# Performance work log

Measured on AMD Instinct MI355X. Metric: run time of the kernel, lower is better.

## Reference

```python
import jax, jax.numpy as jnp
import numpy as np
import math

IN_DIM = 2048
OUT_DIM = 2048
BATCH = 4096
BN_EPS = 1e-5


def setup_inputs() -> dict:
    key = jax.random.key(0)
    ks = jax.random.split(key, 6)
    x = jax.random.normal(ks[0], (BATCH, IN_DIM), dtype=jnp.float32)
    # scale ~ N(1.0, 0.1), translate = 0
    scale = 1.0 + 0.1 * jax.random.normal(ks[1], (1, IN_DIM), dtype=jnp.float32)
    translate = jnp.zeros((1, IN_DIM), dtype=jnp.float32)
    # kaiming-normal-ish init for wave_weight (fan_in), orthogonal-ish for base_weight
    wave_weight = jax.random.normal(ks[2], (OUT_DIM, IN_DIM), dtype=jnp.float32) * np.sqrt(2.0 / IN_DIM)
    bw = jax.random.normal(ks[3], (OUT_DIM, IN_DIM), dtype=jnp.float32)
    q, _ = jnp.linalg.qr(bw.T)  # (IN_DIM, OUT_DIM) orthonormal columns
    base_weight = q.T.astype(jnp.float32)
    gamma = jnp.ones((OUT_DIM,), dtype=jnp.float32)
    beta = jnp.zeros((OUT_DIM,), dtype=jnp.float32)
    return {"x": x, "scale": scale, "translate": translate,
            "wave_weight": wave_weight, "base_weight": base_weight,
            "gamma": gamma, "beta": beta}


def reference(x, scale, translate, wave_weight, base_weight, gamma, beta):
    # Bio wavelet: pi^-1/4 * cos(3u) * exp(-0.5 u^2), u = (x - t) / clamp(s, 1e-3)
    u = (x - translate) / jnp.maximum(scale, 1e-3)            # (B, in)
    wavelet = (math.pi ** -0.25) * jnp.cos(3.0 * u) * jnp.exp(-0.5 * u * u)
    # einsum 'boi,oi->bo' with singleton o broadcast == plain matmul
    wave_out = jnp.einsum('bi,oi->bo', wavelet, wave_weight)  # (B, out)
    base_out = jnp.einsum('bi,oi->bo', x, base_weight)        # (B, out)
    y = wave_out + 0.3 * base_out
    # BatchNorm1d (training mode: batch statistics, biased variance)
    mean = jnp.mean(y, axis=0)
    var = jnp.mean(jnp.square(y - mean), axis=0)
    out = gamma * (y - mean) * jax.lax.rsqrt(var + BN_EPS) + beta
    # dropout treated as identity (deterministic reference)
    return out
```

## Files before the change

### kernel.cpp

```cpp
#include <hip/hip_runtime.h>
#include <stdint.h>

#define IN_DIM 2048
#define OUT_DIM 2048
#define BATCH 4096
#define KDIM (2 * IN_DIM)
#define KROWB (KDIM * 2)
#define KH 2048
#define BN_EPS 1e-5f

typedef __attribute__((ext_vector_type(8))) short bf16x8;
typedef __attribute__((ext_vector_type(4))) float f32x4;

__device__ __forceinline__ unsigned short f2bf(float f) {
  union { float f; unsigned u; } v; v.f = f;
  unsigned r = v.u + 0x7FFFu + ((v.u >> 16) & 1u);
  return (unsigned short)(r >> 16);
}

__global__ void prep_act(const float* __restrict__ x,
                         const float* __restrict__ scale,
                         const float* __restrict__ translate,
                         unsigned short* __restrict__ A) {
  int e = (blockIdx.x * 256 + threadIdx.x) * 4;
  int b = e / IN_DIM;
  int i = e % IN_DIM;
  float4 xv = *(const float4*)(x + e);
  float4 sv = *(const float4*)(scale + i);
  float4 tv = *(const float4*)(translate + i);
  const float c = 0.7511255444649425f;
  float u0 = (xv.x - tv.x) / fmaxf(sv.x, 1e-3f);
  float u1 = (xv.y - tv.y) / fmaxf(sv.y, 1e-3f);
  float u2 = (xv.z - tv.z) / fmaxf(sv.z, 1e-3f);
  float u3 = (xv.w - tv.w) / fmaxf(sv.w, 1e-3f);
  ushort4 wv, xb;
  wv.x = f2bf(c * __cosf(3.0f * u0) * __expf(-0.5f * u0 * u0));
  wv.y = f2bf(c * __cosf(3.0f * u1) * __expf(-0.5f * u1 * u1));
  wv.z = f2bf(c * __cosf(3.0f * u2) * __expf(-0.5f * u2 * u2));
  wv.w = f2bf(c * __cosf(3.0f * u3) * __expf(-0.5f * u3 * u3));
  xb.x = f2bf(xv.x); xb.y = f2bf(xv.y); xb.z = f2bf(xv.z); xb.w = f2bf(xv.w);
  *(ushort4*)(A + (size_t)b * KDIM + i) = wv;
  *(ushort4*)(A + (size_t)b * KDIM + IN_DIM + i) = xb;
}

__global__ void prep_w(const float* __restrict__ ww,
                       const float* __restrict__ bw,
                       unsigned short* __restrict__ W) {
  int e = (blockIdx.x * 256 + threadIdx.x) * 4;
  int o = e / IN_DIM;
  int k = e % IN_DIM;
  float4 a = *(const float4*)(ww + e);
  float4 b = *(const float4*)(bw + e);
  ushort4 wa, wb;
  wa.x = f2bf(a.x); wa.y = f2bf(a.y); wa.z = f2bf(a.z); wa.w = f2bf(a.w);
  wb.x = f2bf(0.3f * b.x); wb.y = f2bf(0.3f * b.y);
  wb.z = f2bf(0.3f * b.z); wb.w = f2bf(0.3f * b.w);
  *(ushort4*)(W + (size_t)o * KDIM + k) = wa;
  *(ushort4*)(W + (size_t)o * KDIM + IN_DIM + k) = wb;
}


#define GLDS(gp, lo) __builtin_amdgcn_global_load_lds( \
    (const __attribute__((address_space(1))) void*)(gp), \
    (__attribute__((address_space(3))) void*)(lds + (lo) + ldsl), 16, 0, 0)

#define MM16(mh) do { \
  __builtin_amdgcn_s_setprio(1); \
  _Pragma("unroll") for (int i2 = 0; i2 < 4; ++i2) \
  _Pragma("unroll") for (int j2 = 0; j2 < 4; ++j2) \
    acc[(mh) * 4 + i2][j2] = __builtin_amdgcn_mfma_f32_16x16x32_bf16( \
        af[i2], bfr[j2], acc[(mh) * 4 + i2][j2], 0, 0, 0); \
  __builtin_amdgcn_s_setprio(0); \
} while (0)

#define LGKM0() asm volatile("s_waitcnt lgkmcnt(0)" ::: "memory")
#define VMW8()  asm volatile("s_waitcnt vmcnt(8)" ::: "memory")
#define VMW4()  asm volatile("s_waitcnt vmcnt(4)" ::: "memory")
#define VMW0()  asm volatile("s_waitcnt vmcnt(0)" ::: "memory")
#define NOW()   do { } while (0)
#define BAR()   do { asm volatile("" ::: "memory"); __builtin_amdgcn_s_barrier(); \
                     asm volatile("" ::: "memory"); } while (0)

#define KT(RS, SS, SOFS, DOST, TAILW) do { \
  const char* Au = lds + ((RS) << 15) + wmOff; \
  const char* Bu = lds + ((RS) << 15) + bnOff; \
  af[0] = *(const bf16x8*)(Au + 0 * 1024 + roff); \
  af[1] = *(const bf16x8*)(Au + 1 * 1024 + roff); \
  af[2] = *(const bf16x8*)(Au + 2 * 1024 + roff); \
  af[3] = *(const bf16x8*)(Au + 3 * 1024 + roff); \
  bfr[0] = *(const bf16x8*)(Bu + 0 * 1024 + roff); \
  bfr[1] = *(const bf16x8*)(Bu + 1 * 1024 + roff); \
  bfr[2] = *(const bf16x8*)(Bu + 2 * 1024 + roff); \
  bfr[3] = *(const bf16x8*)(Bu + 3 * 1024 + roff); \
  if (DOST) { GLDS(a0p + (SOFS), ((SS) << 15) + 0); \
              GLDS(a1p + (SOFS), ((SS) << 15) + 8192); \
              GLDS(b0p + (SOFS), ((SS) << 15) + 16384); \
              GLDS(b1p + (SOFS), ((SS) << 15) + 24576); } \
  MM16(0); \
  af[0] = *(const bf16x8*)(Au + 4 * 1024 + roff); \
  af[1] = *(const bf16x8*)(Au + 5 * 1024 + roff); \
  af[2] = *(const bf16x8*)(Au + 6 * 1024 + roff); \
  af[3] = *(const bf16x8*)(Au + 7 * 1024 + roff); \
  MM16(1); \
  LGKM0(); TAILW; BAR(); \
} while (0)

__global__ __launch_bounds__(512, 2) void gemm256(
    const unsigned short* __restrict__ A,
    const unsigned short* __restrict__ W,
    float* __restrict__ P0, float* __restrict__ P1,
    float* __restrict__ sums, float* __restrict__ sqs) {
  __shared__ char lds[131072];
  const int tid = threadIdx.x;
  const int lane = tid & 63;
  const int wave = tid >> 6;
  const int wm = wave >> 2;
  const int wn = wave & 3;

  const int sw = ((blockIdx.x & 7) << 5) | (blockIdx.x >> 3);
  const int kz = sw >> 7;
  const int brow = ((sw >> 3) & 15) * 256;
  const int bcol = (sw & 7) * 256;
  const size_t kb = (size_t)kz * (KH * 2);

  const int slr = tid >> 3;
  const int srow2 = 2 * slr + ((tid >> 2) & 1);
  const int skslot = (tid & 3) ^ (slr & 3);
  const char* aS0 = (const char*)A + (size_t)(brow + srow2) * KROWB + kb + skslot * 16;
  const char* aS1 = aS0 + (size_t)128 * KROWB;
  const char* bS0 = (const char*)W + (size_t)(bcol + srow2) * KROWB + kb + skslot * 16;
  const char* bS1 = bS0 + (size_t)128 * KROWB;
  const int ldsl = wave * 1024;

  const int lh = (lane & 15) >> 1;
  const int roff = lh * 128 + (lane & 1) * 64 + (((lane >> 4) ^ (lh & 3)) << 4);
  const int wmOff = wm * 8192;
  const int bnOff = 16384 + (wn >> 1) * 8192 + (wn & 1) * 4096;

  f32x4 acc[8][4];
#pragma unroll
  for (int m = 0; m < 8; ++m)
#pragma unroll
    for (int n = 0; n < 4; ++n)
      acc[m][n] = (f32x4){0.f, 0.f, 0.f, 0.f};
  bf16x8 af[4], bfr[4];

  GLDS(aS0, 0); GLDS(aS1, 8192); GLDS(bS0, 16384); GLDS(bS1, 24576);
  GLDS(aS0 + 64, 32768); GLDS(aS1 + 64, 32768 + 8192);
  GLDS(bS0 + 64, 32768 + 16384); GLDS(bS1 + 64, 32768 + 24576);
  GLDS(aS0 + 128, 65536); GLDS(aS1 + 128, 65536 + 8192);
  GLDS(bS0 + 128, 65536 + 16384); GLDS(bS1 + 128, 65536 + 24576);
  VMW8(); BAR();

  const char* a0p = aS0 + 192;
  const char* a1p = aS1 + 192;
  const char* b0p = bS0 + 192;
  const char* b1p = bS1 + 192;

  for (int tt = 0; tt < 60; tt += 4) {
    KT(0, 3, 0,   1, VMW8());
    KT(1, 0, 64,  1, VMW8());
    KT(2, 1, 128, 1, VMW8());
    KT(3, 2, 192, 1, VMW8());
    a0p += 256; a1p += 256; b0p += 256; b1p += 256;
  }
  KT(0, 3, 0, 1, VMW8());
  KT(1, 0, 0, 0, VMW4());
  KT(2, 0, 0, 0, VMW0());
  KT(3, 0, 0, 0, NOW());

  float* Pz = kz ? P1 : P0;
  const int r0 = brow + wm * 128 + (lane >> 4) * 4;
  const int c0 = bcol + wn * 64 + (lane & 15);
#pragma unroll
  for (int m = 0; m < 8; ++m)
#pragma unroll
    for (int n = 0; n < 4; ++n)
#pragma unroll
      for (int j = 0; j < 4; ++j)
        Pz[(size_t)(r0 + m * 16 + j) * OUT_DIM + (c0 + n * 16)] = acc[m][n][j];

  float ps[4], pq[4];
#pragma unroll
  for (int n = 0; n < 4; ++n) {
    float s = 0.f, q = 0.f;
#pragma unroll
    for (int m = 0; m < 8; ++m)
#pragma unroll
      for (int j = 0; j < 4; ++j) {
        float v = acc[m][n][j];
        s += v; q += v * v;
      }
    s += __shfl_xor(s, 16); q += __shfl_xor(q, 16);
    s += __shfl_xor(s, 32); q += __shfl_xor(q, 32);
    ps[n] = s; pq[n] = q;
  }
  if (lane < 16) {
#pragma unroll
    for (int n = 0; n < 4; ++n) {
      atomicAdd(&sums[bcol + wn * 64 + n * 16 + lane], ps[n]);
      atomicAdd(&sqs[bcol + wn * 64 + n * 16 + lane], pq[n]);
    }
  }
}

__global__ void bnorm2(const float* __restrict__ P1, float* __restrict__ Y,
                       const float* __restrict__ sums, const float* __restrict__ sqs,
                       const float* __restrict__ gamma, const float* __restrict__ beta) {
  int e = (blockIdx.x * 256 + threadIdx.x) * 4;
  int c = e % OUT_DIM;
  float4 y = *(float4*)(Y + e);
  float4 p = *(const float4*)(P1 + e);
  y.x += p.x; y.y += p.y; y.z += p.z; y.w += p.w;
  float4 s = *(const float4*)(sums + c);
  float4 q = *(const float4*)(sqs + c);
  float4 g = *(const float4*)(gamma + c);
  float4 bb = *(const float4*)(beta + c);
  const float invB = 1.0f / (float)BATCH;
  float m0 = s.x * invB, m1 = s.y * invB, m2 = s.z * invB, m3 = s.w * invB;
  float i0 = rsqrtf(q.x * invB - m0 * m0 + BN_EPS);
  float i1 = rsqrtf(q.y * invB - m1 * m1 + BN_EPS);
  float i2 = rsqrtf(q.z * invB - m2 * m2 + BN_EPS);
  float i3 = rsqrtf(q.w * invB - m3 * m3 + BN_EPS);
  y.x = g.x * (y.x - m0) * i0 + bb.x;
  y.y = g.y * (y.y - m1) * i1 + bb.y;
  y.z = g.z * (y.z - m2) * i2 + bb.z;
  y.w = g.w * (y.w - m3) * i3 + bb.w;
  *(float4*)(Y + e) = y;
}

extern "C" void kernel_launch(void* const* d_in, const int* in_sizes, int n_in,
                              void* d_out, int out_size, void* d_ws, size_t ws_size,
                              hipStream_t stream) {
  const float* x         = (const float*)d_in[0];
  const float* scale     = (const float*)d_in[1];
  const float* translate = (const float*)d_in[2];
  const float* ww        = (const float*)d_in[3];
  const float* bw        = (const float*)d_in[4];
  const float* gamma     = (const float*)d_in[5];
  const float* beta      = (const float*)d_in[6];
  float* out = (float*)d_out;

  char* ws = (char*)d_ws;
  unsigned short* A = (unsigned short*)ws;
  unsigned short* W = (unsigned short*)(ws + 33554432);
  float* P1   = (float*)(ws + 50331648);
  float* sums = (float*)(ws + 83886080);
  float* sqs  = sums + OUT_DIM;

  hipMemsetAsync(sums, 0, 2 * OUT_DIM * sizeof(float), stream);
  prep_act<<<(BATCH * IN_DIM) / 1024, 256, 0, stream>>>(x, scale, translate, A);
  prep_w<<<(OUT_DIM * IN_DIM) / 1024, 256, 0, stream>>>(ww, bw, W);
  gemm256<<<256, 512, 0, stream>>>(A, W, out, P1, sums, sqs);
  bnorm2<<<(BATCH * OUT_DIM) / 1024, 256, 0, stream>>>(P1, out, sums, sqs, gamma, beta);
}
```

Measured before the change: 109.2 us.

## Split K inside each workgroup and reduce partials in LDS instead of global

Each 512-thread block now covers a 256x128 output tile with two 256-thread halves, each taking half of the K range. The halves are combined through LDS at the end, so the global P1 partial buffer and its extra read in the batch-norm pass go away, saving one 32 MB write and read. The pipeline changes from 4 stages to 3 per half, and LDS use grows to 144 KB. The tile is narrower (128 columns), so each K-step reuses fewer B operands and each half has fewer waves to hide latency.

```diff
diff --git a/kernel.cpp b/kernel.cpp
--- a/kernel.cpp
+++ b/kernel.cpp
@@ -6,7 +6,6 @@
 #define BATCH 4096
 #define KDIM (2 * IN_DIM)
 #define KROWB (KDIM * 2)
-#define KH 2048
 #define BN_EPS 1e-5f
 
 typedef __attribute__((ext_vector_type(8))) short bf16x8;
@@ -62,80 +61,81 @@
 
 #define GLDS(gp, lo) __builtin_amdgcn_global_load_lds( \
     (const __attribute__((address_space(1))) void*)(gp), \
-    (__attribute__((address_space(3))) void*)(lds + (lo) + ldsl), 16, 0, 0)
+    (__attribute__((address_space(3))) void*)(lds + (lo) + ldsw), 16, 0, 0)
 
 #define MM16(mh) do { \
   __builtin_amdgcn_s_setprio(1); \
   _Pragma("unroll") for (int i2 = 0; i2 < 4; ++i2) \
   _Pragma("unroll") for (int j2 = 0; j2 < 4; ++j2) \
     acc[(mh) * 4 + i2][j2] = __builtin_amdgcn_mfma_f32_16x16x32_bf16( \
-        af[i2], bfr[j2], acc[(mh) * 4 + i2][j2], 0, 0, 0); \
+        af[i2], bq[j2], acc[(mh) * 4 + i2][j2], 0, 0, 0); \
   __builtin_amdgcn_s_setprio(0); \
 } while (0)
 
 #define LGKM0() asm volatile("s_waitcnt lgkmcnt(0)" ::: "memory")
-#define VMW8()  asm volatile("s_waitcnt vmcnt(8)" ::: "memory")
-#define VMW4()  asm volatile("s_waitcnt vmcnt(4)" ::: "memory")
+#define VMW6()  asm volatile("s_waitcnt vmcnt(6)" ::: "memory")
 #define VMW0()  asm volatile("s_waitcnt vmcnt(0)" ::: "memory")
 #define NOW()   do { } while (0)
 #define BAR()   do { asm volatile("" ::: "memory"); __builtin_amdgcn_s_barrier(); \
                      asm volatile("" ::: "memory"); } while (0)
 
-#define KT(RS, SS, SOFS, DOST, TAILW) do { \
-  const char* Au = lds + ((RS) << 15) + wmOff; \
-  const char* Bu = lds + ((RS) << 15) + bnOff; \
-  af[0] = *(const bf16x8*)(Au + 0 * 1024 + roff); \
-  af[1] = *(const bf16x8*)(Au + 1 * 1024 + roff); \
-  af[2] = *(const bf16x8*)(Au + 2 * 1024 + roff); \
-  af[3] = *(const bf16x8*)(Au + 3 * 1024 + roff); \
-  bfr[0] = *(const bf16x8*)(Bu + 0 * 1024 + roff); \
-  bfr[1] = *(const bf16x8*)(Bu + 1 * 1024 + roff); \
-  bfr[2] = *(const bf16x8*)(Bu + 2 * 1024 + roff); \
-  bfr[3] = *(const bf16x8*)(Bu + 3 * 1024 + roff); \
-  if (DOST) { GLDS(a0p + (SOFS), ((SS) << 15) + 0); \
-              GLDS(a1p + (SOFS), ((SS) << 15) + 8192); \
-              GLDS(b0p + (SOFS), ((SS) << 15) + 16384); \
-              GLDS(b1p + (SOFS), ((SS) << 15) + 24576); } \
+#define KT(S, SS, TOFS, DOST, TAILW) do { \
+  const char* Lr = lds + gbase + (S) * 24576; \
+  af[0] = *(const bf16x8*)(Lr + aoff + 0 * 1024 + roff); \
+  af[1] = *(const bf16x8*)(Lr + aoff + 1 * 1024 + roff); \
+  af[2] = *(const bf16x8*)(Lr + aoff + 2 * 1024 + roff); \
+  af[3] = *(const bf16x8*)(Lr + aoff + 3 * 1024 + roff); \
+  bq[0] = *(const bf16x8*)(Lr + boff + 0 * 1024 + roff); \
+  bq[1] = *(const bf16x8*)(Lr + boff + 1 * 1024 + roff); \
+  bq[2] = *(const bf16x8*)(Lr + boff + 2 * 1024 + roff); \
+  bq[3] = *(const bf16x8*)(Lr + boff + 3 * 1024 + roff); \
+  if (DOST) { \
+    GLDS(aG + (TOFS),               gbase + (SS) * 24576 + 0); \
+    GLDS(aG + (TOFS) +  64 * KROWB, gbase + (SS) * 24576 + 4096); \
+    GLDS(aG + (TOFS) + 128 * KROWB, gbase + (SS) * 24576 + 8192); \
+    GLDS(aG + (TOFS) + 192 * KROWB, gbase + (SS) * 24576 + 12288); \
+    GLDS(bG + (TOFS),               gbase + (SS) * 24576 + 16384); \
+    GLDS(bG + (TOFS) +  64 * KROWB, gbase + (SS) * 24576 + 20480); \
+  } \
   MM16(0); \
-  af[0] = *(const bf16x8*)(Au + 4 * 1024 + roff); \
-  af[1] = *(const bf16x8*)(Au + 5 * 1024 + roff); \
-  af[2] = *(const bf16x8*)(Au + 6 * 1024 + roff); \
-  af[3] = *(const bf16x8*)(Au + 7 * 1024 + roff); \
+  af[0] = *(const bf16x8*)(Lr + aoff + 4096 + 0 * 1024 + roff); \
+  af[1] = *(const bf16x8*)(Lr + aoff + 4096 + 1 * 1024 + roff); \
+  af[2] = *(const bf16x8*)(Lr + aoff + 4096 + 2 * 1024 + roff); \
+  af[3] = *(const bf16x8*)(Lr + aoff + 4096 + 3 * 1024 + roff); \
   MM16(1); \
   LGKM0(); TAILW; BAR(); \
 } while (0)
 
-__global__ __launch_bounds__(512, 2) void gemm256(
+__global__ __launch_bounds__(512, 2) void gemm_ksplit(
     const unsigned short* __restrict__ A,
     const unsigned short* __restrict__ W,
-    float* __restrict__ P0, float* __restrict__ P1,
+    float* __restrict__ Y,
     float* __restrict__ sums, float* __restrict__ sqs) {
-  __shared__ char lds[131072];
+  __shared__ char lds[147456];
   const int tid = threadIdx.x;
   const int lane = tid & 63;
-  const int wave = tid >> 6;
-  const int wm = wave >> 2;
-  const int wn = wave & 3;
-
-  const int sw = ((blockIdx.x & 7) << 5) | (blockIdx.x >> 3);
-  const int kz = sw >> 7;
-  const int brow = ((sw >> 3) & 15) * 256;
-  const int bcol = (sw & 7) * 256;
-  const size_t kb = (size_t)kz * (KH * 2);
-
-  const int slr = tid >> 3;
-  const int srow2 = 2 * slr + ((tid >> 2) & 1);
-  const int skslot = (tid & 3) ^ (slr & 3);
-  const char* aS0 = (const char*)A + (size_t)(brow + srow2) * KROWB + kb + skslot * 16;
-  const char* aS1 = aS0 + (size_t)128 * KROWB;
-  const char* bS0 = (const char*)W + (size_t)(bcol + srow2) * KROWB + kb + skslot * 16;
-  const char* bS1 = bS0 + (size_t)128 * KROWB;
-  const int ldsl = wave * 1024;
+  const int g = tid >> 8;
+  const int gt = tid & 255;
+  const int w4 = (tid >> 6) & 3;
+  const int wm = w4 >> 1;
+  const int wn = w4 & 1;
+  const int gbase = g * 73728;
+
+  const int xcd = blockIdx.x & 7;
+  const int li = blockIdx.x >> 3;
+  const int brow = ((xcd >> 1) * 4 + (li >> 3)) * 256;
+  const int bcol = ((xcd & 1) * 8 + (li & 7)) * 128;
+
+  const int srow2 = 2 * (gt >> 3) + ((gt >> 2) & 1);
+  const int sksl = (gt & 3) ^ ((gt >> 3) & 3);
+  const char* aG = (const char*)A + (size_t)(brow + srow2) * KROWB + g * 4096 + sksl * 16;
+  const char* bG = (const char*)W + (size_t)(bcol + srow2) * KROWB + g * 4096 + sksl * 16;
+  const int ldsw = w4 * 1024;
 
   const int lh = (lane & 15) >> 1;
   const int roff = lh * 128 + (lane & 1) * 64 + (((lane >> 4) ^ (lh & 3)) << 4);
-  const int wmOff = wm * 8192;
-  const int bnOff = 16384 + (wn >> 1) * 8192 + (wn & 1) * 4096;
+  const int aoff = wm * 8192;
+  const int boff = 16384 + wn * 4096;
 
   f32x4 acc[8][4];
 #pragma unroll
@@ -143,75 +143,82 @@
 #pragma unroll
     for (int n = 0; n < 4; ++n)
       acc[m][n] = (f32x4){0.f, 0.f, 0.f, 0.f};
-  bf16x8 af[4], bfr[4];
-
-  GLDS(aS0, 0); GLDS(aS1, 8192); GLDS(bS0, 16384); GLDS(bS1, 24576);
-  GLDS(aS0 + 64, 32768); GLDS(aS1 + 64, 32768 + 8192);
-  GLDS(bS0 + 64, 32768 + 16384); GLDS(bS1 + 64, 32768 + 24576);
-  GLDS(aS0 + 128, 65536); GLDS(aS1 + 128, 65536 + 8192);
-  GLDS(bS0 + 128, 65536 + 16384); GLDS(bS1 + 128, 65536 + 24576);
-  VMW8(); BAR();
-
-  const char* a0p = aS0 + 192;
-  const char* a1p = aS1 + 192;
-  const char* b0p = bS0 + 192;
-  const char* b1p = bS1 + 192;
-
-  for (int tt = 0; tt < 60; tt += 4) {
-    KT(0, 3, 0,   1, VMW8());
-    KT(1, 0, 64,  1, VMW8());
-    KT(2, 1, 128, 1, VMW8());
-    KT(3, 2, 192, 1, VMW8());
-    a0p += 256; a1p += 256; b0p += 256; b1p += 256;
+  bf16x8 af[4], bq[4];
+
+  GLDS(aG, gbase + 0); GLDS(aG + 64 * KROWB, gbase + 4096);
+  GLDS(aG + 128 * KROWB, gbase + 8192); GLDS(aG + 192 * KROWB, gbase + 12288);
+  GLDS(bG, gbase + 16384); GLDS(bG + 64 * KROWB, gbase + 20480);
+  GLDS(aG + 64, gbase + 24576);
+  GLDS(aG + 64 * KROWB + 64, gbase + 24576 + 4096);
+  GLDS(aG + 128 * KROWB + 64, gbase + 24576 + 8192);
+  GLDS(aG + 192 * KROWB + 64, gbase + 24576 + 12288);
+  GLDS(bG + 64, gbase + 24576 + 16384);
+  GLDS(bG + 64 * KROWB + 64, gbase + 24576 + 20480);
+  VMW6(); BAR();
+
+  for (int tt = 0; tt < 60; tt += 3) {
+    KT(0, 2, (tt + 2) * 64, 1, VMW6());
+    KT(1, 0, (tt + 3) * 64, 1, VMW6());
+    KT(2, 1, (tt + 4) * 64, 1, VMW6());
   }
-  KT(0, 3, 0, 1, VMW8());
-  KT(1, 0, 0, 0, VMW4());
+  KT(0, 2, 62 * 64, 1, VMW6());
+  KT(1, 0, 63 * 64, 1, VMW6());
   KT(2, 0, 0, 0, VMW0());
-  KT(3, 0, 0, 0, NOW());
-
-  float* Pz = kz ? P1 : P0;
-  const int r0 = brow + wm * 128 + (lane >> 4) * 4;
-  const int c0 = bcol + wn * 64 + (lane & 15);
-#pragma unroll
-  for (int m = 0; m < 8; ++m)
-#pragma unroll
-    for (int n = 0; n < 4; ++n)
-#pragma unroll
-      for (int j = 0; j < 4; ++j)
-        Pz[(size_t)(r0 + m * 16 + j) * OUT_DIM + (c0 + n * 16)] = acc[m][n][j];
-
-  float ps[4], pq[4];
-#pragma unroll
-  for (int n = 0; n < 4; ++n) {
-    float s = 0.f, q = 0.f;
+  KT(0, 0, 0, 0, NOW());
+
+  if (g == 1) {
 #pragma unroll
     for (int m = 0; m < 8; ++m)
 #pragma unroll
-      for (int j = 0; j < 4; ++j) {
-        float v = acc[m][n][j];
-        s += v; q += v * v;
+      for (int n = 0; n < 4; ++n)
+        *(f32x4*)(lds + w4 * 32768 + (m * 4 + n) * 1024 + lane * 16) = acc[m][n];
+  }
+  LGKM0(); BAR();
+  if (g == 0) {
+#pragma unroll
+    for (int m = 0; m < 8; ++m)
+#pragma unroll
+      for (int n = 0; n < 4; ++n) {
+        f32x4 p = *(const f32x4*)(lds + w4 * 32768 + (m * 4 + n) * 1024 + lane * 16);
+        acc[m][n] += p;
       }
-    s += __shfl_xor(s, 16); q += __shfl_xor(q, 16);
-    s += __shfl_xor(s, 32); q += __shfl_xor(q, 32);
-    ps[n] = s; pq[n] = q;
-  }
-  if (lane < 16) {
+
+    const int r0 = brow + wm * 128 + (lane >> 4) * 4;
+    const int c0 = bcol + wn * 64 + (lane & 15);
+#pragma unroll
+    for (int m = 0; m < 8; ++m)
+#pragma unroll
+      for (int n = 0; n < 4; ++n)
+#pragma unroll
+        for (int j = 0; j < 4; ++j)
+          Y[(size_t)(r0 + m * 16 + j) * OUT_DIM + (c0 + n * 16)] = acc[m][n][j];
+
 #pragma unroll
     for (int n = 0; n < 4; ++n) {
-      atomicAdd(&sums[bcol + wn * 64 + n * 16 + lane], ps[n]);
-      atomicAdd(&sqs[bcol + wn * 64 + n * 16 + lane], pq[n]);
+      float s = 0.f, q = 0.f;
+#pragma unroll
+      for (int m = 0; m < 8; ++m)
+#pragma unroll
+        for (int j = 0; j < 4; ++j) {
+          float v = acc[m][n][j];
+          s += v; q += v * v;
+        }
+      s += __shfl_xor(s, 16); q += __shfl_xor(q, 16);
+      s += __shfl_xor(s, 32); q += __shfl_xor(q, 32);
+      if (lane < 16) {
+        atomicAdd(&sums[c0 + n * 16], s);
+        atomicAdd(&sqs[c0 + n * 16], q);
+      }
     }
   }
 }
 
-__global__ void bnorm2(const float* __restrict__ P1, float* __restrict__ Y,
-                       const float* __restrict__ sums, const float* __restrict__ sqs,
-                       const float* __restrict__ gamma, const float* __restrict__ beta) {
+__global__ void bnorm(float* __restrict__ Y,
+                      const float* __restrict__ sums, const float* __restrict__ sqs,
+                      const float* __restrict__ gamma, const float* __restrict__ beta) {
   int e = (blockIdx.x * 256 + threadIdx.x) * 4;
   int c = e % OUT_DIM;
   float4 y = *(float4*)(Y + e);
-  float4 p = *(const float4*)(P1 + e);
-  y.x += p.x; y.y += p.y; y.z += p.z; y.w += p.w;
   float4 s = *(const float4*)(sums + c);
   float4 q = *(const float4*)(sqs + c);
   float4 g = *(const float4*)(gamma + c);
@@ -244,13 +251,12 @@
   char* ws = (char*)d_ws;
   unsigned short* A = (unsigned short*)ws;
   unsigned short* W = (unsigned short*)(ws + 33554432);
-  float* P1   = (float*)(ws + 50331648);
-  float* sums = (float*)(ws + 83886080);
+  float* sums = (float*)(ws + 50331648);
   float* sqs  = sums + OUT_DIM;
 
   hipMemsetAsync(sums, 0, 2 * OUT_DIM * sizeof(float), stream);
   prep_act<<<(BATCH * IN_DIM) / 1024, 256, 0, stream>>>(x, scale, translate, A);
   prep_w<<<(OUT_DIM * IN_DIM) / 1024, 256, 0, stream>>>(ww, bw, W);
-  gemm256<<<256, 512, 0, stream>>>(A, W, out, P1, sums, sqs);
-  bnorm2<<<(BATCH * OUT_DIM) / 1024, 256, 0, stream>>>(P1, out, sums, sqs, gamma, beta);
-}
+  gemm_ksplit<<<256, 512, 0, stream>>>(A, W, out, sums, sqs);
+  bnorm<<<(BATCH * OUT_DIM) / 1024, 256, 0, stream>>>(out, sums, sqs, gamma, beta);
+}
```

Result: no change. 110.1 us (+0.8%).
